# Kernel optimization log

Measured on AMD Instinct MI355X. Metric: run time of the kernel, lower is better.

Reference implementation:

```python
import jax, jax.numpy as jnp
import numpy as np

N_NODES = 50000
N_EDGES = 800000
IN_CH, HID_CH, OUT_CH = 128, 256, 128


def _glorot(key, shape):
    fan_in, fan_out = shape[1], shape[0]
    lim = float(np.sqrt(6.0 / (fan_in + fan_out)))
    return jax.random.uniform(key, shape, jnp.float32, -lim, lim)


def setup_inputs() -> dict:
    key = jax.random.key(0)
    ks = jax.random.split(key, 8)
    x = jax.random.normal(ks[0], (N_NODES, IN_CH), jnp.float32)
    edge_index = jax.random.randint(ks[1], (2, N_EDGES), 0, N_NODES, jnp.int64)
    return {
        "x": x,
        "edge_index": edge_index,
        # layer 1: SAGEConv(128 -> 256): lin_l (with bias) on aggregated, lin_r (no bias) on root
        "W1l": _glorot(ks[2], (HID_CH, IN_CH)),
        "b1l": jnp.zeros((HID_CH,), jnp.float32),
        "W1r": _glorot(ks[3], (HID_CH, IN_CH)),
        # layer 2: SAGEConv(256 -> 128)
        "W2l": _glorot(ks[4], (OUT_CH, HID_CH)),
        "b2l": jnp.zeros((OUT_CH,), jnp.float32),
        "W2r": _glorot(ks[5], (OUT_CH, HID_CH)),
    }


def _sage_conv(x, src, dst, Wl, bl, Wr, n_nodes):
    # mean-aggregate neighbor (source) features at destination nodes
    msg = x[src]                                                   # [E, C] gather
    agg = jax.ops.segment_sum(msg, dst, num_segments=n_nodes)      # [N, C]
    deg = jax.ops.segment_sum(jnp.ones((src.shape[0],), x.dtype), dst,
                              num_segments=n_nodes)                # [N]
    mean = agg / jnp.maximum(deg, 1.0)[:, None]                    # zero-degree -> 0
    return mean @ Wl.T + bl + x @ Wr.T


def reference(x, edge_index, W1l, b1l, W1r, W2l, b2l, W2r):
    src, dst = edge_index[0], edge_index[1]
    n = x.shape[0]
    h = _sage_conv(x, src, dst, W1l, b1l, W1r, n)
    h = jax.nn.relu(h)  # dropout is identity in eval mode
    out = _sage_conv(h, src, dst, W2l, b2l, W2r, n)
    return out
```

## Files before the change

kernel.cpp:

```cpp
#include <hip/hip_runtime.h>

#define N_NODES 50000
#define IN_CH   128
#define HID_CH  256
#define OUT_CH  128

#define NB    196
#define NWG   64
#define NBNW  (NB * NWG)

#define LSTR 72

typedef __attribute__((ext_vector_type(8))) short bf16x8;
typedef __attribute__((ext_vector_type(4))) float f32x4;

__device__ __forceinline__ unsigned short f32_bf16_rne(float f) {
    unsigned u = __float_as_uint(f);
    unsigned r = u + 0x7fff + ((u >> 16) & 1);
    return (unsigned short)(r >> 16);
}
__device__ __forceinline__ float bf16lo_f32(unsigned u) { return __uint_as_float(u << 16); }
__device__ __forceinline__ float bf16hi_f32(unsigned u) { return __uint_as_float(u & 0xffff0000u); }

__global__ __launch_bounds__(256) void cvt_bf16_kernel(
    const float* __restrict__ in, unsigned short* __restrict__ outp, int n8)
{
    int i = blockIdx.x * 256 + threadIdx.x;
    if (i >= n8) return;
    const float4* p = reinterpret_cast<const float4*>(in) + 2 * (size_t)i;
    float4 a = p[0], b = p[1];
    alignas(16) unsigned short t[8] = {
        f32_bf16_rne(a.x), f32_bf16_rne(a.y), f32_bf16_rne(a.z), f32_bf16_rne(a.w),
        f32_bf16_rne(b.x), f32_bf16_rne(b.y), f32_bf16_rne(b.z), f32_bf16_rne(b.w)};
    *reinterpret_cast<int4*>(outp + 8 * (size_t)i) = *reinterpret_cast<const int4*>(t);
}

__global__ __launch_bounds__(256) void cvt4_bf16_kernel(
    const float* __restrict__ a0, const float* __restrict__ a1,
    const float* __restrict__ a2, const float* __restrict__ a3,
    unsigned short* __restrict__ o0, unsigned short* __restrict__ o1,
    unsigned short* __restrict__ o2, unsigned short* __restrict__ o3, int per)
{
    int i = blockIdx.x * 256 + threadIdx.x;
    if (i >= 4 * per) return;
    int seg = i / per, j = i - seg * per;
    const float* in = (seg == 0) ? a0 : (seg == 1) ? a1 : (seg == 2) ? a2 : a3;
    unsigned short* outp = (seg == 0) ? o0 : (seg == 1) ? o1 : (seg == 2) ? o2 : o3;
    const float4* p = reinterpret_cast<const float4*>(in) + 2 * (size_t)j;
    float4 a = p[0], b = p[1];
    alignas(16) unsigned short t[8] = {
        f32_bf16_rne(a.x), f32_bf16_rne(a.y), f32_bf16_rne(a.z), f32_bf16_rne(a.w),
        f32_bf16_rne(b.x), f32_bf16_rne(b.y), f32_bf16_rne(b.z), f32_bf16_rne(b.w)};
    *reinterpret_cast<int4*>(outp + 8 * (size_t)j) = *reinterpret_cast<const int4*>(t);
}

__global__ __launch_bounds__(256) void bcount_kernel(
    const int* __restrict__ src, const int* __restrict__ dst,
    int* __restrict__ counts, int E, int chunk)
{
    __shared__ int h[NB];
    const int w = blockIdx.x;
    for (int i = threadIdx.x; i < NB; i += 256) h[i] = 0;
    __syncthreads();
    const int e0 = w * chunk;
    const int e1 = min(e0 + chunk, E);
    for (int e = e0 + threadIdx.x; e < e1; e += 256) {
        int s = src[e], d = dst[e];
        if ((unsigned)s < (unsigned)N_NODES && (unsigned)d < (unsigned)N_NODES)
            atomicAdd(&h[d >> 8], 1);
    }
    __syncthreads();
    for (int i = threadIdx.x; i < NB; i += 256)
        counts[i * NWG + w] = h[i];
}

__global__ __launch_bounds__(256) void scanA_kernel(
    const int* __restrict__ counts, int* __restrict__ S, int* __restrict__ bsum)
{
    __shared__ int s[256];
    int i = blockIdx.x * 256 + threadIdx.x;
    s[threadIdx.x] = (i < NBNW) ? counts[i] : 0;
    __syncthreads();
    for (int off = 1; off < 256; off <<= 1) {
        int t = (threadIdx.x >= off) ? s[threadIdx.x - off] : 0;
        __syncthreads();
        if (threadIdx.x >= off) s[threadIdx.x] += t;
        __syncthreads();
    }
    if (i < NBNW) S[i] = (threadIdx.x == 0) ? 0 : s[threadIdx.x - 1];
    if (threadIdx.x == 0) bsum[blockIdx.x] = s[255];
}

__global__ __launch_bounds__(256) void scanB_kernel(
    const int* __restrict__ bsum, int* __restrict__ boff, int nb)
{
    __shared__ int s[256];
    int v = (threadIdx.x < nb) ? bsum[threadIdx.x] : 0;
    s[threadIdx.x] = v;
    __syncthreads();
    for (int off = 1; off < 256; off <<= 1) {
        int t = (threadIdx.x >= off) ? s[threadIdx.x - off] : 0;
        __syncthreads();
        if (threadIdx.x >= off) s[threadIdx.x] += t;
        __syncthreads();
    }
    if (threadIdx.x < nb)
        boff[threadIdx.x] = (threadIdx.x == 0) ? 0 : s[threadIdx.x - 1];
}

__global__ __launch_bounds__(256) void scanC_kernel(
    int* __restrict__ S, const int* __restrict__ boff,
    const int* __restrict__ counts)
{
    int i = blockIdx.x * 256 + threadIdx.x;
    if (i < NBNW) {
        int r = S[i] + boff[blockIdx.x];
        S[i] = r;
        if (i == NBNW - 1) S[NBNW] = r + counts[i];
    }
}

__global__ __launch_bounds__(256) void bscatter_kernel(
    const int* __restrict__ src, const int* __restrict__ dst,
    const int* __restrict__ S, int2* __restrict__ pairs, int E, int chunk)
{
    __shared__ int cur[NB];
    const int w = blockIdx.x;
    for (int i = threadIdx.x; i < NB; i += 256) cur[i] = S[i * NWG + w];
    __syncthreads();
    const int e0 = w * chunk;
    const int e1 = min(e0 + chunk, E);
    for (int e = e0 + threadIdx.x; e < e1; e += 256) {
        int s = src[e], d = dst[e];
        if ((unsigned)s < (unsigned)N_NODES && (unsigned)d < (unsigned)N_NODES) {
            int pos = atomicAdd(&cur[d >> 8], 1);
            pairs[pos] = make_int2(s, d);
        }
    }
}

__global__ __launch_bounds__(256) void bsort_kernel(
    const int2* __restrict__ pairs, const int* __restrict__ S,
    int* __restrict__ rowptr, int* __restrict__ colidx)
{
    __shared__ int hcnt[256];
    __shared__ int hcur[256];
    const int b = blockIdx.x;
    const int start = S[b * NWG];
    const int endv  = (b == NB - 1) ? S[NBNW] : S[(b + 1) * NWG];

    hcnt[threadIdx.x] = 0;
    __syncthreads();
    for (int e = start + threadIdx.x; e < endv; e += 256)
        atomicAdd(&hcnt[pairs[e].y & 255], 1);
    __syncthreads();
    for (int off = 1; off < 256; off <<= 1) {
        int t = (threadIdx.x >= off) ? hcnt[threadIdx.x - off] : 0;
        __syncthreads();
        if (threadIdx.x >= off) hcnt[threadIdx.x] += t;
        __syncthreads();
    }
    int offv = (threadIdx.x == 0) ? 0 : hcnt[threadIdx.x - 1];
    hcur[threadIdx.x] = offv;
    int node = (b << 8) + threadIdx.x;
    if (node < N_NODES) rowptr[node] = start + offv;
    if (b == NB - 1 && threadIdx.x == 0) rowptr[N_NODES] = endv;
    __syncthreads();
    for (int e = start + threadIdx.x; e < endv; e += 256) {
        int2 p = pairs[e];
        int pos = atomicAdd(&hcur[p.y & 255], 1);
        colidx[start + pos] = p.x;
    }
}

__global__ __launch_bounds__(256) void agg1_kernel(
    const unsigned short* __restrict__ feat, const int* __restrict__ rowptr,
    const int* __restrict__ colidx, unsigned short* __restrict__ outp)
{
    const int node = blockIdx.x * 16 + (threadIdx.x >> 4);
    const int lane = threadIdx.x & 15;
    if (node >= N_NODES) return;
    const int beg = rowptr[node];
    const int end = rowptr[node + 1];

    float acc[8] = {};
    int i = beg;
    for (; i + 1 < end; i += 2) {
        int s0 = colidx[i], s1 = colidx[i + 1];
        int4 v0 = *reinterpret_cast<const int4*>(feat + (size_t)s0 * IN_CH + lane * 8);
        int4 v1 = *reinterpret_cast<const int4*>(feat + (size_t)s1 * IN_CH + lane * 8);
        acc[0] += bf16lo_f32(v0.x); acc[1] += bf16hi_f32(v0.x);
        acc[2] += bf16lo_f32(v0.y); acc[3] += bf16hi_f32(v0.y);
        acc[4] += bf16lo_f32(v0.z); acc[5] += bf16hi_f32(v0.z);
        acc[6] += bf16lo_f32(v0.w); acc[7] += bf16hi_f32(v0.w);
        acc[0] += bf16lo_f32(v1.x); acc[1] += bf16hi_f32(v1.x);
        acc[2] += bf16lo_f32(v1.y); acc[3] += bf16hi_f32(v1.y);
        acc[4] += bf16lo_f32(v1.z); acc[5] += bf16hi_f32(v1.z);
        acc[6] += bf16lo_f32(v1.w); acc[7] += bf16hi_f32(v1.w);
    }
    if (i < end) {
        int s0 = colidx[i];
        int4 v0 = *reinterpret_cast<const int4*>(feat + (size_t)s0 * IN_CH + lane * 8);
        acc[0] += bf16lo_f32(v0.x); acc[1] += bf16hi_f32(v0.x);
        acc[2] += bf16lo_f32(v0.y); acc[3] += bf16hi_f32(v0.y);
        acc[4] += bf16lo_f32(v0.z); acc[5] += bf16hi_f32(v0.z);
        acc[6] += bf16lo_f32(v0.w); acc[7] += bf16hi_f32(v0.w);
    }
    const float sc = 1.0f / fmaxf((float)(end - beg), 1.0f);
    alignas(16) unsigned short t[8];
#pragma unroll
    for (int j = 0; j < 8; ++j) t[j] = f32_bf16_rne(acc[j] * sc);
    *reinterpret_cast<int4*>(outp + (size_t)node * IN_CH + lane * 8) =
        *reinterpret_cast<const int4*>(t);
}

__global__ __launch_bounds__(256) void agg2_kernel(
    const unsigned short* __restrict__ feat, const int* __restrict__ rowptr,
    const int* __restrict__ colidx, float* __restrict__ out)
{
    const int node = blockIdx.x * 16 + (threadIdx.x >> 4);
    const int lane = threadIdx.x & 15;
    if (node >= N_NODES) return;
    const int beg = rowptr[node];
    const int end = rowptr[node + 1];

    float acc[8] = {};
    int i = beg;
    for (; i + 1 < end; i += 2) {
        int s0 = colidx[i], s1 = colidx[i + 1];
        int4 v0 = *reinterpret_cast<const int4*>(feat + (size_t)s0 * OUT_CH + lane * 8);
        int4 v1 = *reinterpret_cast<const int4*>(feat + (size_t)s1 * OUT_CH + lane * 8);
        acc[0] += bf16lo_f32(v0.x); acc[1] += bf16hi_f32(v0.x);
        acc[2] += bf16lo_f32(v0.y); acc[3] += bf16hi_f32(v0.y);
        acc[4] += bf16lo_f32(v0.z); acc[5] += bf16hi_f32(v0.z);
        acc[6] += bf16lo_f32(v0.w); acc[7] += bf16hi_f32(v0.w);
        acc[0] += bf16lo_f32(v1.x); acc[1] += bf16hi_f32(v1.x);
        acc[2] += bf16lo_f32(v1.y); acc[3] += bf16hi_f32(v1.y);
        acc[4] += bf16lo_f32(v1.z); acc[5] += bf16hi_f32(v1.z);
        acc[6] += bf16lo_f32(v1.w); acc[7] += bf16hi_f32(v1.w);
    }
    if (i < end) {
        int s0 = colidx[i];
        int4 v0 = *reinterpret_cast<const int4*>(feat + (size_t)s0 * OUT_CH + lane * 8);
        acc[0] += bf16lo_f32(v0.x); acc[1] += bf16hi_f32(v0.x);
        acc[2] += bf16lo_f32(v0.y); acc[3] += bf16hi_f32(v0.y);
        acc[4] += bf16lo_f32(v0.z); acc[5] += bf16hi_f32(v0.z);
        acc[6] += bf16lo_f32(v0.w); acc[7] += bf16hi_f32(v0.w);
    }
    const float sc = 1.0f / fmaxf((float)(end - beg), 1.0f);
    float* o = out + (size_t)node * OUT_CH + lane * 8;
    float4 o0 = reinterpret_cast<float4*>(o)[0];
    float4 o1 = reinterpret_cast<float4*>(o)[1];
    o0.x += acc[0] * sc; o0.y += acc[1] * sc; o0.z += acc[2] * sc; o0.w += acc[3] * sc;
    o1.x += acc[4] * sc; o1.y += acc[5] * sc; o1.z += acc[6] * sc; o1.w += acc[7] * sc;
    reinterpret_cast<float4*>(o)[0] = o0;
    reinterpret_cast<float4*>(o)[1] = o1;
}

__device__ __forceinline__ void stage64(
    const unsigned short* __restrict__ g, int ldg, int rowBase, int maxRow,
    int kBase, unsigned short* __restrict__ s, int tid)
{
#pragma unroll
    for (int it = 0; it < 4; ++it) {
        int c = tid + it * 256;
        int r = c >> 3;
        int off = (c & 7) * 8;
        int row = rowBase + r;
        if (row >= maxRow) row = maxRow - 1;
        int4 v = *reinterpret_cast<const int4*>(g + (size_t)row * ldg + kBase + off);
        *reinterpret_cast<int4*>(s + r * LSTR + off) = v;
    }
}

__device__ __forceinline__ void mfma_tile(
    const unsigned short* __restrict__ As, const unsigned short* __restrict__ Bs,
    int wm, int wn, int l16, int quad, f32x4 acc[4][4])
{
#pragma unroll
    for (int k0 = 0; k0 < 64; k0 += 32) {
        bf16x8 a[4], b[4];
#pragma unroll
        for (int i = 0; i < 4; ++i)
            a[i] = *reinterpret_cast<const bf16x8*>(
                As + (wm * 64 + i * 16 + l16) * LSTR + k0 + quad * 8);
#pragma unroll
        for (int j = 0; j < 4; ++j)
            b[j] = *reinterpret_cast<const bf16x8*>(
                Bs + (wn * 64 + j * 16 + l16) * LSTR + k0 + quad * 8);
#pragma unroll
        for (int i = 0; i < 4; ++i)
#pragma unroll
            for (int j = 0; j < 4; ++j)
                acc[i][j] = __builtin_amdgcn_mfma_f32_16x16x32_bf16(
                    a[i], b[j], acc[i][j], 0, 0, 0);
    }
}

__global__ __launch_bounds__(256) void gemm1_mfma(
    const unsigned short* __restrict__ mean1b, const unsigned short* __restrict__ xb,
    const unsigned short* __restrict__ W1lb,   const unsigned short* __restrict__ W1rb,
    const float* __restrict__ b1l, unsigned short* __restrict__ hb)
{
    __shared__ unsigned short As[128 * LSTR];
    __shared__ unsigned short Bs[128 * LSTR];
    const int tid = threadIdx.x;
    const int wid = tid >> 6, lane = tid & 63;
    const int wm = wid & 1, wn = wid >> 1;
    const int l16 = lane & 15, quad = lane >> 4;
    const int rowBase = blockIdx.x * 128;
    const int colBase = blockIdx.y * 128;

    f32x4 z = {0.f, 0.f, 0.f, 0.f};
    f32x4 acc[4][4];
#pragma unroll
    for (int i = 0; i < 4; ++i)
#pragma unroll
        for (int j = 0; j < 4; ++j) acc[i][j] = z;

#pragma unroll
    for (int op = 0; op < 2; ++op) {
        const unsigned short* A = op ? xb : mean1b;
        const unsigned short* B = op ? W1rb : W1lb;
#pragma unroll
        for (int kb = 0; kb < IN_CH; kb += 64) {
            __syncthreads();
            stage64(A, IN_CH, rowBase, N_NODES, kb, As, tid);
            stage64(B, IN_CH, colBase, HID_CH, kb, Bs, tid);
            __syncthreads();
            mfma_tile(As, Bs, wm, wn, l16, quad, acc);
        }
    }

#pragma unroll
    for (int j = 0; j < 4; ++j) {
        int col = colBase + wn * 64 + j * 16 + l16;
        float bv = b1l[col];
#pragma unroll
        for (int i = 0; i < 4; ++i) {
            int mBase = rowBase + wm * 64 + i * 16 + quad * 4;
#pragma unroll
            for (int r = 0; r < 4; ++r) {
                int m = mBase + r;
                if (m < N_NODES) {
                    float v = fmaxf(acc[i][j][r] + bv, 0.0f);
                    hb[(size_t)m * HID_CH + col] = f32_bf16_rne(v);
                }
            }
        }
    }
}

__global__ __launch_bounds__(256) void gemm2_mfma(
    const unsigned short* __restrict__ hb, const unsigned short* __restrict__ W2lb,
    const unsigned short* __restrict__ W2rb, const float* __restrict__ b2l,
    unsigned short* __restrict__ pb, float* __restrict__ out)
{
    __shared__ unsigned short As[128 * LSTR];
    __shared__ unsigned short Bs[128 * LSTR];
    const int tid = threadIdx.x;
    const int wid = tid >> 6, lane = tid & 63;
    const int wm = wid & 1, wn = wid >> 1;
    const int l16 = lane & 15, quad = lane >> 4;
    const int rowBase = blockIdx.x * 128;
    const unsigned short* B = blockIdx.y ? W2rb : W2lb;

    f32x4 z = {0.f, 0.f, 0.f, 0.f};
    f32x4 acc[4][4];
#pragma unroll
    for (int i = 0; i < 4; ++i)
#pragma unroll
        for (int j = 0; j < 4; ++j) acc[i][j] = z;

#pragma unroll
    for (int kb = 0; kb < HID_CH; kb += 64) {
        __syncthreads();
        stage64(hb, HID_CH, rowBase, N_NODES, kb, As, tid);
        stage64(B, HID_CH, 0, OUT_CH, kb, Bs, tid);
        __syncthreads();
        mfma_tile(As, Bs, wm, wn, l16, quad, acc);
    }

    if (blockIdx.y == 0) {
#pragma unroll
        for (int j = 0; j < 4; ++j) {
            int col = wn * 64 + j * 16 + l16;
#pragma unroll
            for (int i = 0; i < 4; ++i) {
                int mBase = rowBase + wm * 64 + i * 16 + quad * 4;
#pragma unroll
                for (int r = 0; r < 4; ++r) {
                    int m = mBase + r;
                    if (m < N_NODES)
                        pb[(size_t)m * OUT_CH + col] = f32_bf16_rne(acc[i][j][r]);
                }
            }
        }
    } else {
#pragma unroll
        for (int j = 0; j < 4; ++j) {
            int col = wn * 64 + j * 16 + l16;
            float bv = b2l[col];
#pragma unroll
            for (int i = 0; i < 4; ++i) {
                int mBase = rowBase + wm * 64 + i * 16 + quad * 4;
#pragma unroll
                for (int r = 0; r < 4; ++r) {
                    int m = mBase + r;
                    if (m < N_NODES)
                        out[(size_t)m * OUT_CH + col] = acc[i][j][r] + bv;
                }
            }
        }
    }
}

extern "C" void kernel_launch(void* const* d_in, const int* in_sizes, int n_in,
                              void* d_out, int out_size, void* d_ws, size_t ws_size,
                              hipStream_t stream)
{
    const float* x   = (const float*)d_in[0];
    const int*   ei  = (const int*)d_in[1];
    const float* W1l = (const float*)d_in[2];
    const float* b1l = (const float*)d_in[3];
    const float* W1r = (const float*)d_in[4];
    const float* W2l = (const float*)d_in[5];
    const float* b2l = (const float*)d_in[6];
    const float* W2r = (const float*)d_in[7];

    const int E = in_sizes[1] / 2;
    const int* src = ei;
    const int* dst = ei + E;

    char* ws = (char*)d_ws;
    size_t off = 0;
    auto alloc = [&](size_t bytes) {
        void* p = ws + off;
        off += (bytes + 255) & ~(size_t)255;
        return p;
    };
    unsigned short* xb     = (unsigned short*)alloc((size_t)N_NODES * IN_CH * 2);
    unsigned short* mean1b = (unsigned short*)alloc((size_t)N_NODES * IN_CH * 2);
    unsigned short* hb     = (unsigned short*)alloc((size_t)N_NODES * HID_CH * 2);
    unsigned short* pb     = (unsigned short*)alloc((size_t)N_NODES * OUT_CH * 2);
    unsigned short* W1lb   = (unsigned short*)alloc((size_t)HID_CH * IN_CH * 2);
    unsigned short* W1rb   = (unsigned short*)alloc((size_t)HID_CH * IN_CH * 2);
    unsigned short* W2lb   = (unsigned short*)alloc((size_t)OUT_CH * HID_CH * 2);
    unsigned short* W2rb   = (unsigned short*)alloc((size_t)OUT_CH * HID_CH * 2);
    int*  counts = (int*)alloc((size_t)NBNW * 4);
    int*  S      = (int*)alloc((size_t)(NBNW + 1) * 4);
    int*  bsum   = (int*)alloc((size_t)256 * 4);
    int*  boff   = (int*)alloc((size_t)256 * 4);
    int2* pairs  = (int2*)alloc((size_t)E * 8);
    int*  rowptr = (int*)alloc((size_t)(N_NODES + 1) * 4);
    int*  colidx = (int*)alloc((size_t)E * 4);
    float* out = (float*)d_out;

    const int chunk = (E + NWG - 1) / NWG;
    const int nbS = (NBNW + 255) / 256;

    bcount_kernel<<<NWG, 256, 0, stream>>>(src, dst, counts, E, chunk);
    scanA_kernel<<<nbS, 256, 0, stream>>>(counts, S, bsum);
    scanB_kernel<<<1, 256, 0, stream>>>(bsum, boff, nbS);
    scanC_kernel<<<nbS, 256, 0, stream>>>(S, boff, counts);
    bscatter_kernel<<<NWG, 256, 0, stream>>>(src, dst, S, pairs, E, chunk);
    bsort_kernel<<<NB, 256, 0, stream>>>(pairs, S, rowptr, colidx);

    const int xn8 = N_NODES * IN_CH / 8;
    cvt_bf16_kernel<<<(xn8 + 255) / 256, 256, 0, stream>>>(x, xb, xn8);
    const int wn8 = HID_CH * IN_CH / 8;
    cvt4_bf16_kernel<<<(4 * wn8 + 255) / 256, 256, 0, stream>>>(
        W1l, W1r, W2l, W2r, W1lb, W1rb, W2lb, W2rb, wn8);

    const int aggBlocks = (N_NODES + 15) / 16;
    const int mBlocks = (N_NODES + 127) / 128;

    agg1_kernel<<<aggBlocks, 256, 0, stream>>>(xb, rowptr, colidx, mean1b);
    gemm1_mfma<<<dim3(mBlocks, HID_CH / 128), 256, 0, stream>>>(
        mean1b, xb, W1lb, W1rb, b1l, hb);

    gemm2_mfma<<<dim3(mBlocks, 2), 256, 0, stream>>>(hb, W2lb, W2rb, b2l, pb, out);
    agg2_kernel<<<aggBlocks, 256, 0, stream>>>(pb, rowptr, colidx, out);
}
```

Measured before the change: 260.9 us.

## Fuse prep kernels, single-block scan, pack edge pairs, wider agg and GEMM tiles

Merges the bucket count and the x and weight bf16 conversions into one launch, and replaces the three-kernel scan with a single-block scan. Edge pairs are packed into one 32-bit word to halve scatter and sort traffic. Aggregation now uses a full 64-lane wave per node with four edge groups reduced by shuffles. GEMM1 computes all 256 output columns per block and GEMM2 computes both weight products per block, reusing the staged A tile. The cost is higher register and LDS use in the GEMMs, and the packed pair format assumes source indices fit in 24 bits.

```diff
diff --git a/kernel.cpp b/kernel.cpp
--- a/kernel.cpp
+++ b/kernel.cpp
@@ -8,6 +8,10 @@
 #define NB    196
 #define NWG   64
 #define NBNW  (NB * NWG)
+#define SCHUNK 49
+
+#define XBLK  3125
+#define WBLK  64
 
 #define LSTR 72
 
@@ -22,107 +26,84 @@
 __device__ __forceinline__ float bf16lo_f32(unsigned u) { return __uint_as_float(u << 16); }
 __device__ __forceinline__ float bf16hi_f32(unsigned u) { return __uint_as_float(u & 0xffff0000u); }
 
-__global__ __launch_bounds__(256) void cvt_bf16_kernel(
-    const float* __restrict__ in, unsigned short* __restrict__ outp, int n8)
-{
-    int i = blockIdx.x * 256 + threadIdx.x;
-    if (i >= n8) return;
-    const float4* p = reinterpret_cast<const float4*>(in) + 2 * (size_t)i;
+__device__ __forceinline__ void cvt8(const float* __restrict__ in,
+                                     unsigned short* __restrict__ outp, size_t j)
+{
+    const float4* p = reinterpret_cast<const float4*>(in) + 2 * j;
     float4 a = p[0], b = p[1];
     alignas(16) unsigned short t[8] = {
         f32_bf16_rne(a.x), f32_bf16_rne(a.y), f32_bf16_rne(a.z), f32_bf16_rne(a.w),
         f32_bf16_rne(b.x), f32_bf16_rne(b.y), f32_bf16_rne(b.z), f32_bf16_rne(b.w)};
-    *reinterpret_cast<int4*>(outp + 8 * (size_t)i) = *reinterpret_cast<const int4*>(t);
-}
-
-__global__ __launch_bounds__(256) void cvt4_bf16_kernel(
-    const float* __restrict__ a0, const float* __restrict__ a1,
-    const float* __restrict__ a2, const float* __restrict__ a3,
-    unsigned short* __restrict__ o0, unsigned short* __restrict__ o1,
-    unsigned short* __restrict__ o2, unsigned short* __restrict__ o3, int per)
-{
-    int i = blockIdx.x * 256 + threadIdx.x;
-    if (i >= 4 * per) return;
-    int seg = i / per, j = i - seg * per;
-    const float* in = (seg == 0) ? a0 : (seg == 1) ? a1 : (seg == 2) ? a2 : a3;
-    unsigned short* outp = (seg == 0) ? o0 : (seg == 1) ? o1 : (seg == 2) ? o2 : o3;
-    const float4* p = reinterpret_cast<const float4*>(in) + 2 * (size_t)j;
-    float4 a = p[0], b = p[1];
-    alignas(16) unsigned short t[8] = {
-        f32_bf16_rne(a.x), f32_bf16_rne(a.y), f32_bf16_rne(a.z), f32_bf16_rne(a.w),
-        f32_bf16_rne(b.x), f32_bf16_rne(b.y), f32_bf16_rne(b.z), f32_bf16_rne(b.w)};
-    *reinterpret_cast<int4*>(outp + 8 * (size_t)j) = *reinterpret_cast<const int4*>(t);
-}
-
-__global__ __launch_bounds__(256) void bcount_kernel(
+    *reinterpret_cast<int4*>(outp + 8 * j) = *reinterpret_cast<const int4*>(t);
+}
+
+__global__ __launch_bounds__(256) void prep_kernel(
     const int* __restrict__ src, const int* __restrict__ dst,
-    int* __restrict__ counts, int E, int chunk)
-{
-    __shared__ int h[NB];
-    const int w = blockIdx.x;
-    for (int i = threadIdx.x; i < NB; i += 256) h[i] = 0;
-    __syncthreads();
-    const int e0 = w * chunk;
-    const int e1 = min(e0 + chunk, E);
-    for (int e = e0 + threadIdx.x; e < e1; e += 256) {
-        int s = src[e], d = dst[e];
-        if ((unsigned)s < (unsigned)N_NODES && (unsigned)d < (unsigned)N_NODES)
-            atomicAdd(&h[d >> 8], 1);
-    }
-    __syncthreads();
-    for (int i = threadIdx.x; i < NB; i += 256)
-        counts[i * NWG + w] = h[i];
-}
-
-__global__ __launch_bounds__(256) void scanA_kernel(
-    const int* __restrict__ counts, int* __restrict__ S, int* __restrict__ bsum)
-{
-    __shared__ int s[256];
-    int i = blockIdx.x * 256 + threadIdx.x;
-    s[threadIdx.x] = (i < NBNW) ? counts[i] : 0;
+    int* __restrict__ counts, int E, int chunk,
+    const float* __restrict__ x, unsigned short* __restrict__ xb,
+    const float* __restrict__ W1l, const float* __restrict__ W1r,
+    const float* __restrict__ W2l, const float* __restrict__ W2r,
+    unsigned short* __restrict__ W1lb, unsigned short* __restrict__ W1rb,
+    unsigned short* __restrict__ W2lb, unsigned short* __restrict__ W2rb)
+{
+    const int b = blockIdx.x;
+    if (b < NWG) {
+        __shared__ int h[NB];
+        for (int i = threadIdx.x; i < NB; i += 256) h[i] = 0;
+        __syncthreads();
+        const int e0 = b * chunk;
+        const int e1 = min(e0 + chunk, E);
+        for (int e = e0 + threadIdx.x; e < e1; e += 256) {
+            int s = src[e], d = dst[e];
+            if ((unsigned)s < (unsigned)N_NODES && (unsigned)d < (unsigned)N_NODES)
+                atomicAdd(&h[d >> 8], 1);
+        }
+        __syncthreads();
+        for (int i = threadIdx.x; i < NB; i += 256)
+            counts[i * NWG + b] = h[i];
+    } else if (b < NWG + XBLK) {
+        size_t j = (size_t)(b - NWG) * 256 + threadIdx.x;
+        cvt8(x, xb, j);
+    } else {
+        int idx = (b - NWG - XBLK) * 256 + threadIdx.x;
+        int seg = idx >> 12, j = idx & 4095;
+        const float* in = (seg == 0) ? W1l : (seg == 1) ? W1r : (seg == 2) ? W2l : W2r;
+        unsigned short* o = (seg == 0) ? W1lb : (seg == 1) ? W1rb : (seg == 2) ? W2lb : W2rb;
+        cvt8(in, o, (size_t)j);
+    }
+}
+
+__global__ __launch_bounds__(256) void scan_all_kernel(
+    const int* __restrict__ counts, int* __restrict__ S)
+{
+    __shared__ int tot[256];
+    const int t = threadIdx.x;
+    const int base = t * SCHUNK;
+    int loc[SCHUNK];
+    int sum = 0;
+#pragma unroll
+    for (int k = 0; k < SCHUNK; ++k) {
+        loc[k] = sum;
+        sum += counts[base + k];
+    }
+    tot[t] = sum;
     __syncthreads();
     for (int off = 1; off < 256; off <<= 1) {
-        int t = (threadIdx.x >= off) ? s[threadIdx.x - off] : 0;
-        __syncthreads();
-        if (threadIdx.x >= off) s[threadIdx.x] += t;
-        __syncthreads();
-    }
-    if (i < NBNW) S[i] = (threadIdx.x == 0) ? 0 : s[threadIdx.x - 1];
-    if (threadIdx.x == 0) bsum[blockIdx.x] = s[255];
-}
-
-__global__ __launch_bounds__(256) void scanB_kernel(
-    const int* __restrict__ bsum, int* __restrict__ boff, int nb)
-{
-    __shared__ int s[256];
-    int v = (threadIdx.x < nb) ? bsum[threadIdx.x] : 0;
-    s[threadIdx.x] = v;
-    __syncthreads();
-    for (int off = 1; off < 256; off <<= 1) {
-        int t = (threadIdx.x >= off) ? s[threadIdx.x - off] : 0;
-        __syncthreads();
-        if (threadIdx.x >= off) s[threadIdx.x] += t;
-        __syncthreads();
-    }
-    if (threadIdx.x < nb)
-        boff[threadIdx.x] = (threadIdx.x == 0) ? 0 : s[threadIdx.x - 1];
-}
-
-__global__ __launch_bounds__(256) void scanC_kernel(
-    int* __restrict__ S, const int* __restrict__ boff,
-    const int* __restrict__ counts)
-{
-    int i = blockIdx.x * 256 + threadIdx.x;
-    if (i < NBNW) {
-        int r = S[i] + boff[blockIdx.x];
-        S[i] = r;
-        if (i == NBNW - 1) S[NBNW] = r + counts[i];
-    }
+        int v = (t >= off) ? tot[t - off] : 0;
+        __syncthreads();
+        if (t >= off) tot[t] += v;
+        __syncthreads();
+    }
+    int offv = (t == 0) ? 0 : tot[t - 1];
+#pragma unroll
+    for (int k = 0; k < SCHUNK; ++k)
+        S[base + k] = loc[k] + offv;
+    if (t == 255) S[NBNW] = offv + sum;
 }
 
 __global__ __launch_bounds__(256) void bscatter_kernel(
     const int* __restrict__ src, const int* __restrict__ dst,
-    const int* __restrict__ S, int2* __restrict__ pairs, int E, int chunk)
+    const int* __restrict__ S, int* __restrict__ pairs, int E, int chunk)
 {
     __shared__ int cur[NB];
     const int w = blockIdx.x;
@@ -134,13 +115,13 @@
         int s = src[e], d = dst[e];
         if ((unsigned)s < (unsigned)N_NODES && (unsigned)d < (unsigned)N_NODES) {
             int pos = atomicAdd(&cur[d >> 8], 1);
-            pairs[pos] = make_int2(s, d);
+            pairs[pos] = (s << 8) | (d & 255);
         }
     }
 }
 
 __global__ __launch_bounds__(256) void bsort_kernel(
-    const int2* __restrict__ pairs, const int* __restrict__ S,
+    const int* __restrict__ pairs, const int* __restrict__ S,
     int* __restrict__ rowptr, int* __restrict__ colidx)
 {
     __shared__ int hcnt[256];
@@ -152,7 +133,7 @@
     hcnt[threadIdx.x] = 0;
     __syncthreads();
     for (int e = start + threadIdx.x; e < endv; e += 256)
-        atomicAdd(&hcnt[pairs[e].y & 255], 1);
+        atomicAdd(&hcnt[pairs[e] & 255], 1);
     __syncthreads();
     for (int off = 1; off < 256; off <<= 1) {
         int t = (threadIdx.x >= off) ? hcnt[threadIdx.x - off] : 0;
@@ -167,102 +148,85 @@
     if (b == NB - 1 && threadIdx.x == 0) rowptr[N_NODES] = endv;
     __syncthreads();
     for (int e = start + threadIdx.x; e < endv; e += 256) {
-        int2 p = pairs[e];
-        int pos = atomicAdd(&hcur[p.y & 255], 1);
-        colidx[start + pos] = p.x;
-    }
-}
+        int p = pairs[e];
+        int pos = atomicAdd(&hcur[p & 255], 1);
+        colidx[start + pos] = (unsigned)p >> 8;
+    }
+}
+
+#define AGG_BODY(CH)                                                            \
+    const int node = blockIdx.x * 4 + (threadIdx.x >> 6);                       \
+    if (node >= N_NODES) return;                                                \
+    const int lane = threadIdx.x & 63;                                          \
+    const int grp = lane >> 4, ch = lane & 15;                                  \
+    const int beg = rowptr[node], end = rowptr[node + 1];                       \
+    float acc[8] = {};                                                          \
+    int i = beg + grp;                                                          \
+    for (; i + 4 < end; i += 8) {                                               \
+        int s0 = colidx[i], s1 = colidx[i + 4];                                 \
+        int4 v0 = *reinterpret_cast<const int4*>(feat + (size_t)s0 * CH + ch * 8); \
+        int4 v1 = *reinterpret_cast<const int4*>(feat + (size_t)s1 * CH + ch * 8); \
+        acc[0] += bf16lo_f32(v0.x); acc[1] += bf16hi_f32(v0.x);                 \
+        acc[2] += bf16lo_f32(v0.y); acc[3] += bf16hi_f32(v0.y);                 \
+        acc[4] += bf16lo_f32(v0.z); acc[5] += bf16hi_f32(v0.z);                 \
+        acc[6] += bf16lo_f32(v0.w); acc[7] += bf16hi_f32(v0.w);                 \
+        acc[0] += bf16lo_f32(v1.x); acc[1] += bf16hi_f32(v1.x);                 \
+        acc[2] += bf16lo_f32(v1.y); acc[3] += bf16hi_f32(v1.y);                 \
+        acc[4] += bf16lo_f32(v1.z); acc[5] += bf16hi_f32(v1.z);                 \
+        acc[6] += bf16lo_f32(v1.w); acc[7] += bf16hi_f32(v1.w);                 \
+    }                                                                           \
+    if (i < end) {                                                              \
+        int s0 = colidx[i];                                                     \
+        int4 v0 = *reinterpret_cast<const int4*>(feat + (size_t)s0 * CH + ch * 8); \
+        acc[0] += bf16lo_f32(v0.x); acc[1] += bf16hi_f32(v0.x);                 \
+        acc[2] += bf16lo_f32(v0.y); acc[3] += bf16hi_f32(v0.y);                 \
+        acc[4] += bf16lo_f32(v0.z); acc[5] += bf16hi_f32(v0.z);                 \
+        acc[6] += bf16lo_f32(v0.w); acc[7] += bf16hi_f32(v0.w);                 \
+    }                                                                           \
+    _Pragma("unroll")                                                           \
+    for (int j = 0; j < 8; ++j) {                                               \
+        acc[j] += __shfl_xor(acc[j], 16);                                       \
+        acc[j] += __shfl_xor(acc[j], 32);                                       \
+    }                                                                           \
+    const float sc = 1.0f / fmaxf((float)(end - beg), 1.0f);
 
 __global__ __launch_bounds__(256) void agg1_kernel(
     const unsigned short* __restrict__ feat, const int* __restrict__ rowptr,
     const int* __restrict__ colidx, unsigned short* __restrict__ outp)
 {
-    const int node = blockIdx.x * 16 + (threadIdx.x >> 4);
-    const int lane = threadIdx.x & 15;
-    if (node >= N_NODES) return;
-    const int beg = rowptr[node];
-    const int end = rowptr[node + 1];
-
-    float acc[8] = {};
-    int i = beg;
-    for (; i + 1 < end; i += 2) {
-        int s0 = colidx[i], s1 = colidx[i + 1];
-        int4 v0 = *reinterpret_cast<const int4*>(feat + (size_t)s0 * IN_CH + lane * 8);
-        int4 v1 = *reinterpret_cast<const int4*>(feat + (size_t)s1 * IN_CH + lane * 8);
-        acc[0] += bf16lo_f32(v0.x); acc[1] += bf16hi_f32(v0.x);
-        acc[2] += bf16lo_f32(v0.y); acc[3] += bf16hi_f32(v0.y);
-        acc[4] += bf16lo_f32(v0.z); acc[5] += bf16hi_f32(v0.z);
-        acc[6] += bf16lo_f32(v0.w); acc[7] += bf16hi_f32(v0.w);
-        acc[0] += bf16lo_f32(v1.x); acc[1] += bf16hi_f32(v1.x);
-        acc[2] += bf16lo_f32(v1.y); acc[3] += bf16hi_f32(v1.y);
-        acc[4] += bf16lo_f32(v1.z); acc[5] += bf16hi_f32(v1.z);
-        acc[6] += bf16lo_f32(v1.w); acc[7] += bf16hi_f32(v1.w);
-    }
-    if (i < end) {
-        int s0 = colidx[i];
-        int4 v0 = *reinterpret_cast<const int4*>(feat + (size_t)s0 * IN_CH + lane * 8);
-        acc[0] += bf16lo_f32(v0.x); acc[1] += bf16hi_f32(v0.x);
-        acc[2] += bf16lo_f32(v0.y); acc[3] += bf16hi_f32(v0.y);
-        acc[4] += bf16lo_f32(v0.z); acc[5] += bf16hi_f32(v0.z);
-        acc[6] += bf16lo_f32(v0.w); acc[7] += bf16hi_f32(v0.w);
-    }
-    const float sc = 1.0f / fmaxf((float)(end - beg), 1.0f);
-    alignas(16) unsigned short t[8];
-#pragma unroll
-    for (int j = 0; j < 8; ++j) t[j] = f32_bf16_rne(acc[j] * sc);
-    *reinterpret_cast<int4*>(outp + (size_t)node * IN_CH + lane * 8) =
-        *reinterpret_cast<const int4*>(t);
+    AGG_BODY(IN_CH)
+    if (grp == 0) {
+        alignas(16) unsigned short t[8];
+#pragma unroll
+        for (int j = 0; j < 8; ++j) t[j] = f32_bf16_rne(acc[j] * sc);
+        *reinterpret_cast<int4*>(outp + (size_t)node * IN_CH + ch * 8) =
+            *reinterpret_cast<const int4*>(t);
+    }
 }
 
 __global__ __launch_bounds__(256) void agg2_kernel(
     const unsigned short* __restrict__ feat, const int* __restrict__ rowptr,
     const int* __restrict__ colidx, float* __restrict__ out)
 {
-    const int node = blockIdx.x * 16 + (threadIdx.x >> 4);
-    const int lane = threadIdx.x & 15;
-    if (node >= N_NODES) return;
-    const int beg = rowptr[node];
-    const int end = rowptr[node + 1];
-
-    float acc[8] = {};
-    int i = beg;
-    for (; i + 1 < end; i += 2) {
-        int s0 = colidx[i], s1 = colidx[i + 1];
-        int4 v0 = *reinterpret_cast<const int4*>(feat + (size_t)s0 * OUT_CH + lane * 8);
-        int4 v1 = *reinterpret_cast<const int4*>(feat + (size_t)s1 * OUT_CH + lane * 8);
-        acc[0] += bf16lo_f32(v0.x); acc[1] += bf16hi_f32(v0.x);
-        acc[2] += bf16lo_f32(v0.y); acc[3] += bf16hi_f32(v0.y);
-        acc[4] += bf16lo_f32(v0.z); acc[5] += bf16hi_f32(v0.z);
-        acc[6] += bf16lo_f32(v0.w); acc[7] += bf16hi_f32(v0.w);
-        acc[0] += bf16lo_f32(v1.x); acc[1] += bf16hi_f32(v1.x);
-        acc[2] += bf16lo_f32(v1.y); acc[3] += bf16hi_f32(v1.y);
-        acc[4] += bf16lo_f32(v1.z); acc[5] += bf16hi_f32(v1.z);
-        acc[6] += bf16lo_f32(v1.w); acc[7] += bf16hi_f32(v1.w);
-    }
-    if (i < end) {
-        int s0 = colidx[i];
-        int4 v0 = *reinterpret_cast<const int4*>(feat + (size_t)s0 * OUT_CH + lane * 8);
-        acc[0] += bf16lo_f32(v0.x); acc[1] += bf16hi_f32(v0.x);
-        acc[2] += bf16lo_f32(v0.y); acc[3] += bf16hi_f32(v0.y);
-        acc[4] += bf16lo_f32(v0.z); acc[5] += bf16hi_f32(v0.z);
-        acc[6] += bf16lo_f32(v0.w); acc[7] += bf16hi_f32(v0.w);
-    }
-    const float sc = 1.0f / fmaxf((float)(end - beg), 1.0f);
-    float* o = out + (size_t)node * OUT_CH + lane * 8;
-    float4 o0 = reinterpret_cast<float4*>(o)[0];
-    float4 o1 = reinterpret_cast<float4*>(o)[1];
-    o0.x += acc[0] * sc; o0.y += acc[1] * sc; o0.z += acc[2] * sc; o0.w += acc[3] * sc;
-    o1.x += acc[4] * sc; o1.y += acc[5] * sc; o1.z += acc[6] * sc; o1.w += acc[7] * sc;
-    reinterpret_cast<float4*>(o)[0] = o0;
-    reinterpret_cast<float4*>(o)[1] = o1;
-}
-
-__device__ __forceinline__ void stage64(
+    AGG_BODY(OUT_CH)
+    if (grp == 0) {
+        float* o = out + (size_t)node * OUT_CH + ch * 8;
+        float4 o0 = reinterpret_cast<float4*>(o)[0];
+        float4 o1 = reinterpret_cast<float4*>(o)[1];
+        o0.x += acc[0] * sc; o0.y += acc[1] * sc; o0.z += acc[2] * sc; o0.w += acc[3] * sc;
+        o1.x += acc[4] * sc; o1.y += acc[5] * sc; o1.z += acc[6] * sc; o1.w += acc[7] * sc;
+        reinterpret_cast<float4*>(o)[0] = o0;
+        reinterpret_cast<float4*>(o)[1] = o1;
+    }
+}
+
+template <int ROWS>
+__device__ __forceinline__ void stageT(
     const unsigned short* __restrict__ g, int ldg, int rowBase, int maxRow,
     int kBase, unsigned short* __restrict__ s, int tid)
 {
 #pragma unroll
-    for (int it = 0; it < 4; ++it) {
+    for (int it = 0; it < ROWS / 32; ++it) {
         int c = tid + it * 256;
         int r = c >> 3;
         int off = (c & 7) * 8;
@@ -273,50 +237,25 @@
     }
 }
 
-__device__ __forceinline__ void mfma_tile(
-    const unsigned short* __restrict__ As, const unsigned short* __restrict__ Bs,
-    int wm, int wn, int l16, int quad, f32x4 acc[4][4])
-{
-#pragma unroll
-    for (int k0 = 0; k0 < 64; k0 += 32) {
-        bf16x8 a[4], b[4];
-#pragma unroll
-        for (int i = 0; i < 4; ++i)
-            a[i] = *reinterpret_cast<const bf16x8*>(
-                As + (wm * 64 + i * 16 + l16) * LSTR + k0 + quad * 8);
-#pragma unroll
-        for (int j = 0; j < 4; ++j)
-            b[j] = *reinterpret_cast<const bf16x8*>(
-                Bs + (wn * 64 + j * 16 + l16) * LSTR + k0 + quad * 8);
-#pragma unroll
-        for (int i = 0; i < 4; ++i)
-#pragma unroll
-            for (int j = 0; j < 4; ++j)
-                acc[i][j] = __builtin_amdgcn_mfma_f32_16x16x32_bf16(
-                    a[i], b[j], acc[i][j], 0, 0, 0);
-    }
-}
-
 __global__ __launch_bounds__(256) void gemm1_mfma(
     const unsigned short* __restrict__ mean1b, const unsigned short* __restrict__ xb,
     const unsigned short* __restrict__ W1lb,   const unsigned short* __restrict__ W1rb,
     const float* __restrict__ b1l, unsigned short* __restrict__ hb)
 {
     __shared__ unsigned short As[128 * LSTR];
-    __shared__ unsigned short Bs[128 * LSTR];
+    __shared__ unsigned short Bs[256 * LSTR];
     const int tid = threadIdx.x;
     const int wid = tid >> 6, lane = tid & 63;
     const int wm = wid & 1, wn = wid >> 1;
     const int l16 = lane & 15, quad = lane >> 4;
     const int rowBase = blockIdx.x * 128;
-    const int colBase = blockIdx.y * 128;
 
     f32x4 z = {0.f, 0.f, 0.f, 0.f};
-    f32x4 acc[4][4];
+    f32x4 acc[4][8];
 #pragma unroll
     for (int i = 0; i < 4; ++i)
 #pragma unroll
-        for (int j = 0; j < 4; ++j) acc[i][j] = z;
+        for (int j = 0; j < 8; ++j) acc[i][j] = z;
 
 #pragma unroll
     for (int op = 0; op < 2; ++op) {
@@ -325,16 +264,33 @@
 #pragma unroll
         for (int kb = 0; kb < IN_CH; kb += 64) {
             __syncthreads();
-            stage64(A, IN_CH, rowBase, N_NODES, kb, As, tid);
-            stage64(B, IN_CH, colBase, HID_CH, kb, Bs, tid);
+            stageT<128>(A, IN_CH, rowBase, N_NODES, kb, As, tid);
+            stageT<256>(B, IN_CH, 0, HID_CH, kb, Bs, tid);
             __syncthreads();
-            mfma_tile(As, Bs, wm, wn, l16, quad, acc);
-        }
-    }
-
-#pragma unroll
-    for (int j = 0; j < 4; ++j) {
-        int col = colBase + wn * 64 + j * 16 + l16;
+#pragma unroll
+            for (int k0 = 0; k0 < 64; k0 += 32) {
+                bf16x8 a[4], b[8];
+#pragma unroll
+                for (int i = 0; i < 4; ++i)
+                    a[i] = *reinterpret_cast<const bf16x8*>(
+                        As + (wm * 64 + i * 16 + l16) * LSTR + k0 + quad * 8);
+#pragma unroll
+                for (int j = 0; j < 8; ++j)
+                    b[j] = *reinterpret_cast<const bf16x8*>(
+                        Bs + (wn * 128 + j * 16 + l16) * LSTR + k0 + quad * 8);
+#pragma unroll
+                for (int i = 0; i < 4; ++i)
+#pragma unroll
+                    for (int j = 0; j < 8; ++j)
+                        acc[i][j] = __builtin_amdgcn_mfma_f32_16x16x32_bf16(
+                            a[i], b[j], acc[i][j], 0, 0, 0);
+            }
+        }
+    }
+
+#pragma unroll
+    for (int j = 0; j < 8; ++j) {
+        int col = wn * 128 + j * 16 + l16;
         float bv = b1l[col];
 #pragma unroll
         for (int i = 0; i < 4; ++i) {
@@ -357,58 +313,67 @@
     unsigned short* __restrict__ pb, float* __restrict__ out)
 {
     __shared__ unsigned short As[128 * LSTR];
-    __shared__ unsigned short Bs[128 * LSTR];
+    __shared__ unsigned short Bl[128 * LSTR];
+    __shared__ unsigned short Br[128 * LSTR];
     const int tid = threadIdx.x;
     const int wid = tid >> 6, lane = tid & 63;
     const int wm = wid & 1, wn = wid >> 1;
     const int l16 = lane & 15, quad = lane >> 4;
     const int rowBase = blockIdx.x * 128;
-    const unsigned short* B = blockIdx.y ? W2rb : W2lb;
 
     f32x4 z = {0.f, 0.f, 0.f, 0.f};
-    f32x4 acc[4][4];
+    f32x4 accl[4][4], accr[4][4];
 #pragma unroll
     for (int i = 0; i < 4; ++i)
 #pragma unroll
-        for (int j = 0; j < 4; ++j) acc[i][j] = z;
+        for (int j = 0; j < 4; ++j) { accl[i][j] = z; accr[i][j] = z; }
 
 #pragma unroll
     for (int kb = 0; kb < HID_CH; kb += 64) {
         __syncthreads();
-        stage64(hb, HID_CH, rowBase, N_NODES, kb, As, tid);
-        stage64(B, HID_CH, 0, OUT_CH, kb, Bs, tid);
-        __syncthreads();
-        mfma_tile(As, Bs, wm, wn, l16, quad, acc);
-    }
-
-    if (blockIdx.y == 0) {
-#pragma unroll
-        for (int j = 0; j < 4; ++j) {
-            int col = wn * 64 + j * 16 + l16;
-#pragma unroll
-            for (int i = 0; i < 4; ++i) {
-                int mBase = rowBase + wm * 64 + i * 16 + quad * 4;
-#pragma unroll
-                for (int r = 0; r < 4; ++r) {
-                    int m = mBase + r;
-                    if (m < N_NODES)
-                        pb[(size_t)m * OUT_CH + col] = f32_bf16_rne(acc[i][j][r]);
+        stageT<128>(hb,   HID_CH, rowBase, N_NODES, kb, As, tid);
+        stageT<128>(W2lb, HID_CH, 0, OUT_CH, kb, Bl, tid);
+        stageT<128>(W2rb, HID_CH, 0, OUT_CH, kb, Br, tid);
+        __syncthreads();
+#pragma unroll
+        for (int k0 = 0; k0 < 64; k0 += 32) {
+            bf16x8 a[4], bl[4], br[4];
+#pragma unroll
+            for (int i = 0; i < 4; ++i)
+                a[i] = *reinterpret_cast<const bf16x8*>(
+                    As + (wm * 64 + i * 16 + l16) * LSTR + k0 + quad * 8);
+#pragma unroll
+            for (int j = 0; j < 4; ++j) {
+                bl[j] = *reinterpret_cast<const bf16x8*>(
+                    Bl + (wn * 64 + j * 16 + l16) * LSTR + k0 + quad * 8);
+                br[j] = *reinterpret_cast<const bf16x8*>(
+                    Br + (wn * 64 + j * 16 + l16) * LSTR + k0 + quad * 8);
+            }
+#pragma unroll
+            for (int i = 0; i < 4; ++i)
+#pragma unroll
+                for (int j = 0; j < 4; ++j) {
+                    accl[i][j] = __builtin_amdgcn_mfma_f32_16x16x32_bf16(
+                        a[i], bl[j], accl[i][j], 0, 0, 0);
+                    accr[i][j] = __builtin_amdgcn_mfma_f32_16x16x32_bf16(
+                        a[i], br[j], accr[i][j], 0, 0, 0);
                 }
-            }
-        }
-    } else {
-#pragma unroll
-        for (int j = 0; j < 4; ++j) {
-            int col = wn * 64 + j * 16 + l16;
-            float bv = b2l[col];
-#pragma unroll
-            for (int i = 0; i < 4; ++i) {
-                int mBase = rowBase + wm * 64 + i * 16 + quad * 4;
-#pragma unroll
-                for (int r = 0; r < 4; ++r) {
-                    int m = mBase + r;
-                    if (m < N_NODES)
-                        out[(size_t)m * OUT_CH + col] = acc[i][j][r] + bv;
+        }
+    }
+
+#pragma unroll
+    for (int j = 0; j < 4; ++j) {
+        int col = wn * 64 + j * 16 + l16;
+        float bv = b2l[col];
+#pragma unroll
+        for (int i = 0; i < 4; ++i) {
+            int mBase = rowBase + wm * 64 + i * 16 + quad * 4;
+#pragma unroll
+            for (int r = 0; r < 4; ++r) {
+                int m = mBase + r;
+                if (m < N_NODES) {
+                    pb[(size_t)m * OUT_CH + col] = f32_bf16_rne(accl[i][j][r]);
+                    out[(size_t)m * OUT_CH + col] = accr[i][j][r] + bv;
                 }
             }
         }
@@ -447,38 +412,27 @@
     unsigned short* W1rb   = (unsigned short*)alloc((size_t)HID_CH * IN_CH * 2);
     unsigned short* W2lb   = (unsigned short*)alloc((size_t)OUT_CH * HID_CH * 2);
     unsigned short* W2rb   = (unsigned short*)alloc((size_t)OUT_CH * HID_CH * 2);
-    int*  counts = (int*)alloc((size_t)NBNW * 4);
-    int*  S      = (int*)alloc((size_t)(NBNW + 1) * 4);
-    int*  bsum   = (int*)alloc((size_t)256 * 4);
-    int*  boff   = (int*)alloc((size_t)256 * 4);
-    int2* pairs  = (int2*)alloc((size_t)E * 8);
-    int*  rowptr = (int*)alloc((size_t)(N_NODES + 1) * 4);
-    int*  colidx = (int*)alloc((size_t)E * 4);
+    int* counts = (int*)alloc((size_t)NBNW * 4);
+    int* S      = (int*)alloc((size_t)(NBNW + 1) * 4);
+    int* pairs  = (int*)alloc((size_t)E * 4);
+    int* rowptr = (int*)alloc((size_t)(N_NODES + 1) * 4);
+    int* colidx = (int*)alloc((size_t)E * 4);
     float* out = (float*)d_out;
 
     const int chunk = (E + NWG - 1) / NWG;
-    const int nbS = (NBNW + 255) / 256;
-
-    bcount_kernel<<<NWG, 256, 0, stream>>>(src, dst, counts, E, chunk);
-    scanA_kernel<<<nbS, 256, 0, stream>>>(counts, S, bsum);
-    scanB_kernel<<<1, 256, 0, stream>>>(bsum, boff, nbS);
-    scanC_kernel<<<nbS, 256, 0, stream>>>(S, boff, counts);
+
+    prep_kernel<<<NWG + XBLK + WBLK, 256, 0, stream>>>(
+        src, dst, counts, E, chunk, x, xb,
+        W1l, W1r, W2l, W2r, W1lb, W1rb, W2lb, W2rb);
+    scan_all_kernel<<<1, 256, 0, stream>>>(counts, S);
     bscatter_kernel<<<NWG, 256, 0, stream>>>(src, dst, S, pairs, E, chunk);
     bsort_kernel<<<NB, 256, 0, stream>>>(pairs, S, rowptr, colidx);
 
-    const int xn8 = N_NODES * IN_CH / 8;
-    cvt_bf16_kernel<<<(xn8 + 255) / 256, 256, 0, stream>>>(x, xb, xn8);
-    const int wn8 = HID_CH * IN_CH / 8;
-    cvt4_bf16_kernel<<<(4 * wn8 + 255) / 256, 256, 0, stream>>>(
-        W1l, W1r, W2l, W2r, W1lb, W1rb, W2lb, W2rb, wn8);
-
-    const int aggBlocks = (N_NODES + 15) / 16;
+    const int aggBlocks = (N_NODES + 3) / 4;
     const int mBlocks = (N_NODES + 127) / 128;
 
     agg1_kernel<<<aggBlocks, 256, 0, stream>>>(xb, rowptr, colidx, mean1b);
-    gemm1_mfma<<<dim3(mBlocks, HID_CH / 128), 256, 0, stream>>>(
-        mean1b, xb, W1lb, W1rb, b1l, hb);
-
-    gemm2_mfma<<<dim3(mBlocks, 2), 256, 0, stream>>>(hb, W2lb, W2rb, b2l, pb, out);
+    gemm1_mfma<<<mBlocks, 256, 0, stream>>>(mean1b, xb, W1lb, W1rb, b1l, hb);
+    gemm2_mfma<<<mBlocks, 256, 0, stream>>>(hb, W2lb, W2rb, b2l, pb, out);
     agg2_kernel<<<aggBlocks, 256, 0, stream>>>(pb, rowptr, colidx, out);
 }
```

After: 313.4 us. +20.1%, slower.
